# Kernel tuning notes

Hardware: AMD Instinct MI355X
Metric: run time of the kernel (lower is better)

Reference implementation:

```python
import jax, jax.numpy as jnp
import numpy as np

N_NODES = 100000
N_EDGES = 6400000
NUM_FEATURES = 128
NUM_CLASSES = 10


def _gcn_norm(edge_index, num_nodes):
    # PyG GCNConv default: add self-loops, symmetric normalization
    src, dst = edge_index[0], edge_index[1]
    loop = jnp.arange(num_nodes, dtype=src.dtype)
    src = jnp.concatenate([src, loop])
    dst = jnp.concatenate([dst, loop])
    deg = jax.ops.segment_sum(jnp.ones_like(dst, dtype=jnp.float32), dst,
                              num_segments=num_nodes)
    dinv = jnp.where(deg > 0, jax.lax.rsqrt(deg), 0.0)
    norm = dinv[src] * dinv[dst]  # [E + N]
    return src, dst, norm


def _gcn_conv(x, W, b, src, dst, norm, num_nodes):
    h = x @ W                              # [N, out] small feature matmul
    msg = h[src] * norm[:, None]           # gather + per-edge scale
    agg = jax.ops.segment_sum(msg, dst, num_segments=num_nodes)  # scatter-add
    return agg + b


def setup_inputs() -> dict:
    key = jax.random.key(0)
    ks = jax.random.split(key, 10)
    x = jax.random.normal(ks[0], (N_NODES, NUM_FEATURES), dtype=jnp.float32)
    edge_index = jax.random.randint(ks[1], (2, N_EDGES), 0, N_NODES, dtype=jnp.int64)

    def glorot(k, shape):
        lim = np.sqrt(6.0 / (shape[0] + shape[1]))
        return jax.random.uniform(k, shape, jnp.float32, -lim, lim)

    return {
        "x": x,
        "edge_index": edge_index,
        "W1": glorot(ks[2], (NUM_FEATURES, 4)), "b1": jnp.zeros((4,), jnp.float32),
        "W2": glorot(ks[3], (4, 4)),            "b2": jnp.zeros((4,), jnp.float32),
        "W3": glorot(ks[4], (4, 2)),            "b3": jnp.zeros((2,), jnp.float32),
        "Wc": glorot(ks[5], (2, NUM_CLASSES)),  "bc": jnp.zeros((NUM_CLASSES,), jnp.float32),
    }


def reference(x, edge_index, W1, b1, W2, b2, W3, b3, Wc, bc):
    num_nodes = x.shape[0]
    src, dst, norm = _gcn_norm(edge_index, num_nodes)
    h = jnp.tanh(_gcn_conv(x, W1, b1, src, dst, norm, num_nodes))
    h = jnp.tanh(_gcn_conv(h, W2, b2, src, dst, norm, num_nodes))
    h = jnp.tanh(_gcn_conv(h, W3, b3, src, dst, norm, num_nodes))
    out = h @ Wc + bc
    return out, h
```

## Files before the change

### kernel.cpp

```cpp
#include <hip/hip_runtime.h>
#include <hip/hip_bf16.h>
#include <stdint.h>

#define N_NODES 100000
#define N_EDGES 6400000

#define NPB 128
#define NBKT 782
#define CAP 10752
#define SORT_CAP 9216
#define OUT_CAP (SORT_CAP + NPB * 3)
#define BIN_CHUNK 8192
#define BIN_THREADS 512
#define BIN_ITER (BIN_CHUNK / BIN_THREADS)
#define SORT_THREADS 512
#define SORT_V4 5
#define NBIN_BLOCKS ((N_EDGES + BIN_CHUNK - 1) / BIN_CHUNK)


__device__ __forceinline__ void make_rec(unsigned s, unsigned d,
                                         unsigned& rec, short& bb) {
  if (s < N_NODES && d < N_NODES) {
    bb = (short)(d >> 7);
    rec = s | ((d & (NPB - 1u)) << 17) | (((d >> 7) & 255u) << 24);
  }
}

__global__ __launch_bounds__(512) void k_bin(const void* __restrict__ ei,
                                             int* __restrict__ gcur,
                                             unsigned* __restrict__ perm1) {
  __shared__ unsigned staging[BIN_CHUNK];
  __shared__ int lcnt[1024];
  __shared__ int wsum[8];
  __shared__ int s_tot;
  __shared__ int s_th[3];
  __shared__ int s_is64;
  int t = threadIdx.x;
  lcnt[t] = 0; lcnt[t + 512] = 0;
  if (t < 64) {
    unsigned hv = ((const unsigned*)ei)[2 * t + 1];
    unsigned long long m = __ballot(hv != 0u);
    if (t == 0) s_is64 = (m == 0ull);
  }
  __syncthreads();
  int is64 = s_is64;
  size_t e0 = (size_t)blockIdx.x * BIN_CHUNK;
  int n = (int)(((e0 + BIN_CHUNK) <= N_EDGES) ? BIN_CHUNK : (N_EDGES - e0));

  unsigned rec[BIN_ITER];
  short bb[BIN_ITER];
  short rnk[BIN_ITER];
#pragma unroll
  for (int i = 0; i < BIN_ITER; ++i) { rec[i] = 0xFFFFFFFFu; bb[i] = 0; }

  if (is64) {
    const long long* e = (const long long*)ei;
#pragma unroll
    for (int i = 0; i < BIN_ITER / 2; ++i) {
      int k = 2 * t + 1024 * i;
      if (k < n) {
        uint4 sp = *(const uint4*)(e + e0 + k);
        uint4 dp = *(const uint4*)(e + (size_t)N_EDGES + e0 + k);
        make_rec(sp.x, dp.x, rec[2 * i], bb[2 * i]);
        make_rec(sp.z, dp.z, rec[2 * i + 1], bb[2 * i + 1]);
      }
    }
  } else {
    const unsigned* e = (const unsigned*)ei;
#pragma unroll
    for (int i = 0; i < BIN_ITER / 4; ++i) {
      int k = 4 * t + 2048 * i;
      if (k < n) {
        uint4 sq = *(const uint4*)(e + e0 + k);
        uint4 dq = *(const uint4*)(e + (size_t)N_EDGES + e0 + k);
        make_rec(sq.x, dq.x, rec[4 * i],     bb[4 * i]);
        make_rec(sq.y, dq.y, rec[4 * i + 1], bb[4 * i + 1]);
        make_rec(sq.z, dq.z, rec[4 * i + 2], bb[4 * i + 2]);
        make_rec(sq.w, dq.w, rec[4 * i + 3], bb[4 * i + 3]);
      }
    }
  }
#pragma unroll
  for (int i = 0; i < BIN_ITER; ++i) {
    rnk[i] = 0;
    if (rec[i] != 0xFFFFFFFFu)
      rnk[i] = (short)atomicAdd(&lcnt[bb[i]], 1);
  }
  __syncthreads();
  int c0 = lcnt[2 * t], c1 = lcnt[2 * t + 1];
  int s = c0 + c1;
  int lane = t & 63, w = t >> 6;
  int incl = s;
#pragma unroll
  for (int o = 1; o < 64; o <<= 1) {
    int u = __shfl_up(incl, o);
    if (lane >= o) incl += u;
  }
  if (lane == 63) wsum[w] = incl;
  __syncthreads();
  int wb = 0;
  for (int i = 0; i < w; ++i) wb += wsum[i];
  int excl0 = wb + incl - s;
  int excl1 = excl0 + c0;
  lcnt[2 * t] = excl0; lcnt[2 * t + 1] = excl1;
  if (t == 128) s_th[0] = excl0;
  if (t == 256) s_th[1] = excl0;
  if (t == 384) s_th[2] = excl0;
  if (t == 511) s_tot = excl1 + c1;
  int gb0 = c0 ? atomicAdd(&gcur[2 * t], c0) : 0;
  int gb1 = c1 ? atomicAdd(&gcur[2 * t + 1], c1) : 0;
  __syncthreads();
#pragma unroll
  for (int i = 0; i < BIN_ITER; ++i) {
    if (rec[i] != 0xFFFFFFFFu) {
      int p = lcnt[bb[i]] + rnk[i];
      staging[p] = rec[i];
    }
  }
  __syncthreads();
  lcnt[2 * t] = gb0 - excl0;
  lcnt[2 * t + 1] = gb1 - excl1;
  __syncthreads();
  int tot = s_tot, th0 = s_th[0], th1 = s_th[1], th2 = s_th[2];
  for (int j = t; j < tot; j += 512) {
    unsigned r = staging[j];
    int hi = (j >= th0) + (j >= th1) + (j >= th2);
    int b = (int)(r >> 24) | (hi << 8);
    int o = lcnt[b] + j;
    if (o < CAP) perm1[(size_t)b * CAP + o] = r;
  }
}

__global__ __launch_bounds__(512) void k_sort(const int* __restrict__ gcur,
                                              const unsigned* __restrict__ perm1,
                                              unsigned* __restrict__ perm2,
                                              int2* __restrict__ offdeg,
                                              float* __restrict__ dinv) {
  __shared__ __align__(16) unsigned outbuf[OUT_CAP];
  __shared__ int h[NPB];
  __shared__ int wsum2[2];
  __shared__ int s_tot;
  int b = blockIdx.x, t = threadIdx.x;
  if (t < NPB) h[t] = 0;
  __syncthreads();
  int cnt = min(gcur[b], SORT_CAP);
  int base = b * CAP;
  unsigned rec[4 * SORT_V4];
  short rnk[4 * SORT_V4];
#pragma unroll
  for (int i = 0; i < SORT_V4; ++i) {
    int j = 4 * t + 2048 * i;
    uint4 q = *(const uint4*)(perm1 + base + j);
    rec[4 * i]     = (j     < cnt) ? q.x : 0xFFFFFFFFu;
    rec[4 * i + 1] = (j + 1 < cnt) ? q.y : 0xFFFFFFFFu;
    rec[4 * i + 2] = (j + 2 < cnt) ? q.z : 0xFFFFFFFFu;
    rec[4 * i + 3] = (j + 3 < cnt) ? q.w : 0xFFFFFFFFu;
  }
#pragma unroll
  for (int i = 0; i < 4 * SORT_V4; ++i) {
    rnk[i] = 0;
    if (rec[i] != 0xFFFFFFFFu)
      rnk[i] = (short)atomicAdd(&h[(rec[i] >> 17) & (NPB - 1)], 1);
  }
  __syncthreads();
  int degb = 0, degs4 = 0, incl = 0;
  if (t < NPB) {
    degb = h[t];
    degs4 = (degb + 3) & ~3;
    incl = degs4;
    int lane = t & 63;
#pragma unroll
    for (int o = 1; o < 64; o <<= 1) {
      int u = __shfl_up(incl, o);
      if (lane >= o) incl += u;
    }
    if (lane == 63) wsum2[t >> 6] = incl;
  }
  __syncthreads();
  int excl4 = 0;
  if (t < NPB) {
    excl4 = (t >= 64 ? wsum2[0] : 0) + incl - degs4;
    int node = b * NPB + t;
    if (node < N_NODES) {
      offdeg[node] = make_int2(base + excl4, degb);
      float dd = (float)degb + 1.0f;
      float y = rsqrtf(dd);
      y = y * (1.5f - 0.5f * dd * y * y);
      dinv[node] = y;
    }
    if (t == NPB - 1) s_tot = excl4 + degs4;
  }
  __syncthreads();
  if (t < NPB) h[t] = excl4;
  __syncthreads();
#pragma unroll
  for (int i = 0; i < 4 * SORT_V4; ++i) {
    if (rec[i] != 0xFFFFFFFFu)
      outbuf[h[(rec[i] >> 17) & (NPB - 1)] + rnk[i]] = rec[i] & 0x1FFFF;
  }
  __syncthreads();
  int tot = s_tot;
#pragma unroll
  for (int i = 0; i < SORT_V4; ++i) {
    int j = 4 * t + 2048 * i;
    if (j < tot)
      *(uint4*)(perm2 + base + j) = *(const uint4*)(outbuf + j);
  }
}

__global__ __launch_bounds__(256) void k_mm1(const float* __restrict__ x,
                                             const float* __restrict__ W1,
                                             const float* __restrict__ dinv,
                                             float* __restrict__ hs1) {
  int gid = blockIdx.x * blockDim.x + threadIdx.x;
  int node = gid >> 6;
  int lane = threadIdx.x & 63;
  if (node >= N_NODES) return;
  float2 v = ((const float2*)x)[(size_t)node * 64 + lane];
  float4 w0 = ((const float4*)W1)[2 * lane];
  float4 w1 = ((const float4*)W1)[2 * lane + 1];
  float a0 = v.x * w0.x + v.y * w1.x;
  float a1 = v.x * w0.y + v.y * w1.y;
  float a2 = v.x * w0.z + v.y * w1.z;
  float a3 = v.x * w0.w + v.y * w1.w;
#pragma unroll
  for (int off = 32; off > 0; off >>= 1) {
    a0 += __shfl_down(a0, off);
    a1 += __shfl_down(a1, off);
    a2 += __shfl_down(a2, off);
    a3 += __shfl_down(a3, off);
  }
  if (lane == 0) {
    float d = dinv[node];
    ((float4*)hs1)[node] = make_float4(d * a0, d * a1, d * a2, d * a3);
  }
}


__global__ __launch_bounds__(256) void k_l1(const int2* __restrict__ offdeg,
                                            const unsigned* __restrict__ perm2,
                                            const float* __restrict__ hs1,
                                            const float* __restrict__ dinv,
                                            const float* __restrict__ W2,
                                            const float* __restrict__ b1,
                                            float* __restrict__ hs2) {
  int node = blockIdx.x * 16 + (threadIdx.x >> 4);
  int l = threadIdx.x & 15;
  int2 od = offdeg[node];
  int base = od.x, d = od.y;
  float a0 = 0, a1 = 0, a2 = 0, a3 = 0;
  for (int j = 4 * l; j + 4 <= d; j += 64) {
    uint4 s = *(const uint4*)(perm2 + base + j);
    float4 v0 = ((const float4*)hs1)[s.x];
    float4 v1 = ((const float4*)hs1)[s.y];
    float4 v2 = ((const float4*)hs1)[s.z];
    float4 v3 = ((const float4*)hs1)[s.w];
    a0 += v0.x + v1.x + v2.x + v3.x;
    a1 += v0.y + v1.y + v2.y + v3.y;
    a2 += v0.z + v1.z + v2.z + v3.z;
    a3 += v0.w + v1.w + v2.w + v3.w;
  }
  int rb = d & ~3;
  if (l < d - rb) {
    float4 v = ((const float4*)hs1)[perm2[base + rb + l]];
    a0 += v.x; a1 += v.y; a2 += v.z; a3 += v.w;
  }
#pragma unroll
  for (int o = 8; o > 0; o >>= 1) {
    a0 += __shfl_down(a0, o); a1 += __shfl_down(a1, o);
    a2 += __shfl_down(a2, o); a3 += __shfl_down(a3, o);
  }
  if (l == 0) {
    float dn = dinv[node];
    float4 hl = ((const float4*)hs1)[node];
    float t0 = tanhf(dn * (a0 + hl.x) + b1[0]);
    float t1 = tanhf(dn * (a1 + hl.y) + b1[1]);
    float t2 = tanhf(dn * (a2 + hl.z) + b1[2]);
    float t3 = tanhf(dn * (a3 + hl.w) + b1[3]);
    float4 r;
    r.x = dn * (t0 * W2[0] + t1 * W2[4] + t2 * W2[8]  + t3 * W2[12]);
    r.y = dn * (t0 * W2[1] + t1 * W2[5] + t2 * W2[9]  + t3 * W2[13]);
    r.z = dn * (t0 * W2[2] + t1 * W2[6] + t2 * W2[10] + t3 * W2[14]);
    r.w = dn * (t0 * W2[3] + t1 * W2[7] + t2 * W2[11] + t3 * W2[15]);
    ((float4*)hs2)[node] = r;
  }
}

__global__ __launch_bounds__(256) void k_l2(const int2* __restrict__ offdeg,
                                            const unsigned* __restrict__ perm2,
                                            const float* __restrict__ hs2,
                                            const float* __restrict__ dinv,
                                            const float* __restrict__ W3,
                                            const float* __restrict__ b2,
                                            float* __restrict__ hs3) {
  int node = blockIdx.x * 16 + (threadIdx.x >> 4);
  int l = threadIdx.x & 15;
  int2 od = offdeg[node];
  int base = od.x, d = od.y;
  float a0 = 0, a1 = 0, a2 = 0, a3 = 0;
  for (int j = 4 * l; j + 4 <= d; j += 64) {
    uint4 s = *(const uint4*)(perm2 + base + j);
    float4 v0 = ((const float4*)hs2)[s.x];
    float4 v1 = ((const float4*)hs2)[s.y];
    float4 v2 = ((const float4*)hs2)[s.z];
    float4 v3 = ((const float4*)hs2)[s.w];
    a0 += v0.x + v1.x + v2.x + v3.x;
    a1 += v0.y + v1.y + v2.y + v3.y;
    a2 += v0.z + v1.z + v2.z + v3.z;
    a3 += v0.w + v1.w + v2.w + v3.w;
  }
  int rb = d & ~3;
  if (l < d - rb) {
    float4 v = ((const float4*)hs2)[perm2[base + rb + l]];
    a0 += v.x; a1 += v.y; a2 += v.z; a3 += v.w;
  }
#pragma unroll
  for (int o = 8; o > 0; o >>= 1) {
    a0 += __shfl_down(a0, o); a1 += __shfl_down(a1, o);
    a2 += __shfl_down(a2, o); a3 += __shfl_down(a3, o);
  }
  if (l == 0) {
    float dn = dinv[node];
    float4 hl = ((const float4*)hs2)[node];
    float t0 = tanhf(dn * (a0 + hl.x) + b2[0]);
    float t1 = tanhf(dn * (a1 + hl.y) + b2[1]);
    float t2 = tanhf(dn * (a2 + hl.z) + b2[2]);
    float t3 = tanhf(dn * (a3 + hl.w) + b2[3]);
    float2 r;
    r.x = dn * (t0 * W3[0] + t1 * W3[2] + t2 * W3[4] + t3 * W3[6]);
    r.y = dn * (t0 * W3[1] + t1 * W3[3] + t2 * W3[5] + t3 * W3[7]);
    ((float2*)hs3)[node] = r;
  }
}

__global__ __launch_bounds__(256) void k_l3(const int2* __restrict__ offdeg,
                                            const unsigned* __restrict__ perm2,
                                            const float* __restrict__ hs3,
                                            const float* __restrict__ dinv,
                                            const float* __restrict__ Wc,
                                            const float* __restrict__ bc,
                                            const float* __restrict__ b3,
                                            float* __restrict__ out) {
  int node = blockIdx.x * 16 + (threadIdx.x >> 4);
  int l = threadIdx.x & 15;
  int2 od = offdeg[node];
  int base = od.x, d = od.y;
  float a0 = 0, a1 = 0;
  for (int j = 4 * l; j + 4 <= d; j += 64) {
    uint4 s = *(const uint4*)(perm2 + base + j);
    float2 v0 = ((const float2*)hs3)[s.x];
    float2 v1 = ((const float2*)hs3)[s.y];
    float2 v2 = ((const float2*)hs3)[s.z];
    float2 v3 = ((const float2*)hs3)[s.w];
    a0 += v0.x + v1.x + v2.x + v3.x;
    a1 += v0.y + v1.y + v2.y + v3.y;
  }
  int rb = d & ~3;
  if (l < d - rb) {
    float2 v = ((const float2*)hs3)[perm2[base + rb + l]];
    a0 += v.x; a1 += v.y;
  }
#pragma unroll
  for (int o = 8; o > 0; o >>= 1) {
    a0 += __shfl_xor(a0, o); a1 += __shfl_xor(a1, o);
  }
  float dn = dinv[node];
  float2 hl = ((const float2*)hs3)[node];
  float t0 = tanhf(dn * (a0 + hl.x) + b3[0]);
  float t1 = tanhf(dn * (a1 + hl.y) + b3[1]);
  if (l < 10)
    out[(size_t)node * 10 + l] = t0 * Wc[l] + t1 * Wc[10 + l] + bc[l];
  else if (l == 10)
    out[(size_t)N_NODES * 10 + 2 * node + 0] = t0;
  else if (l == 11)
    out[(size_t)N_NODES * 10 + 2 * node + 1] = t1;
}

extern "C" void kernel_launch(void* const* d_in, const int* in_sizes, int n_in,
                              void* d_out, int out_size, void* d_ws, size_t ws_size,
                              hipStream_t stream) {
  const float* x  = (const float*)d_in[0];
  const void*  ei = d_in[1];
  const float* W1 = (const float*)d_in[2];
  const float* b1 = (const float*)d_in[3];
  const float* W2 = (const float*)d_in[4];
  const float* b2 = (const float*)d_in[5];
  const float* W3 = (const float*)d_in[6];
  const float* b3 = (const float*)d_in[7];
  const float* Wc = (const float*)d_in[8];
  const float* bc = (const float*)d_in[9];
  float* out = (float*)d_out;

  const size_t N = N_NODES;
  float* base = (float*)d_ws;
  float* dinv = base;
  float* hs1  = base + N;
  float* hs2  = base + 5 * N;
  float* hs3  = base + 9 * N;
  int2*  offdeg = (int2*)(base + 11 * N);
  int*   gcur = (int*)(base + 13 * N);
  unsigned* perm1 = (unsigned*)(base + 13 * N + 2048);
  unsigned* perm2 = perm1 + (size_t)NBKT * CAP;

  hipMemsetAsync(gcur, 0, 1024 * sizeof(int), stream);
  k_bin<<<NBIN_BLOCKS, BIN_THREADS, 0, stream>>>(ei, gcur, perm1);
  k_sort<<<NBKT, SORT_THREADS, 0, stream>>>(gcur, perm1, perm2, offdeg, dinv);
  k_mm1<<<(N_NODES * 64) / 256, 256, 0, stream>>>(x, W1, dinv, hs1);

  const int LB = N_NODES / 16;
  k_l1<<<LB, 256, 0, stream>>>(offdeg, perm2, hs1, dinv, W2, b1, hs2);
  k_l2<<<LB, 256, 0, stream>>>(offdeg, perm2, hs2, dinv, W3, b2, hs3);
  k_l3<<<LB, 256, 0, stream>>>(offdeg, perm2, hs3, dinv, Wc, bc, b3, out);
}
```

Before: 301.3 us.

## Halve bin chunk, pack rank into bucket word, and re-read perm1 in sort

Halves BIN_CHUNK so k_bin uses less shared memory and runs more blocks, and packs the local rank into the upper bits of the bucket index to save registers. Both kernels get a minimum-blocks hint in launch_bounds. k_sort no longer holds records and ranks in registers; it reads perm1 twice, once for the histogram and once for the scatter, and places records with atomicAdd on the offset counters. This trades extra global reads and an order-dependent placement within each node for lower register pressure and higher occupancy.

New measurement: 325.1 us. 1.08x slower.

```diff
diff --git a/kernel.cpp b/kernel.cpp
--- a/kernel.cpp
+++ b/kernel.cpp
@@ -10,7 +10,7 @@
 #define CAP 10752
 #define SORT_CAP 9216
 #define OUT_CAP (SORT_CAP + NPB * 3)
-#define BIN_CHUNK 8192
+#define BIN_CHUNK 4096
 #define BIN_THREADS 512
 #define BIN_ITER (BIN_CHUNK / BIN_THREADS)
 #define SORT_THREADS 512
@@ -19,16 +19,16 @@
 
 
 __device__ __forceinline__ void make_rec(unsigned s, unsigned d,
-                                         unsigned& rec, short& bb) {
+                                         unsigned& rec, int& pk) {
   if (s < N_NODES && d < N_NODES) {
-    bb = (short)(d >> 7);
+    pk = (int)(d >> 7);
     rec = s | ((d & (NPB - 1u)) << 17) | (((d >> 7) & 255u) << 24);
   }
 }
 
-__global__ __launch_bounds__(512) void k_bin(const void* __restrict__ ei,
-                                             int* __restrict__ gcur,
-                                             unsigned* __restrict__ perm1) {
+__global__ __launch_bounds__(512, 8) void k_bin(const void* __restrict__ ei,
+                                                int* __restrict__ gcur,
+                                                unsigned* __restrict__ perm1) {
   __shared__ unsigned staging[BIN_CHUNK];
   __shared__ int lcnt[1024];
   __shared__ int wsum[8];
@@ -48,10 +48,9 @@
   int n = (int)(((e0 + BIN_CHUNK) <= N_EDGES) ? BIN_CHUNK : (N_EDGES - e0));
 
   unsigned rec[BIN_ITER];
-  short bb[BIN_ITER];
-  short rnk[BIN_ITER];
-#pragma unroll
-  for (int i = 0; i < BIN_ITER; ++i) { rec[i] = 0xFFFFFFFFu; bb[i] = 0; }
+  int pk[BIN_ITER];
+#pragma unroll
+  for (int i = 0; i < BIN_ITER; ++i) { rec[i] = 0xFFFFFFFFu; pk[i] = 0; }
 
   if (is64) {
     const long long* e = (const long long*)ei;
@@ -61,8 +60,8 @@
       if (k < n) {
         uint4 sp = *(const uint4*)(e + e0 + k);
         uint4 dp = *(const uint4*)(e + (size_t)N_EDGES + e0 + k);
-        make_rec(sp.x, dp.x, rec[2 * i], bb[2 * i]);
-        make_rec(sp.z, dp.z, rec[2 * i + 1], bb[2 * i + 1]);
+        make_rec(sp.x, dp.x, rec[2 * i],     pk[2 * i]);
+        make_rec(sp.z, dp.z, rec[2 * i + 1], pk[2 * i + 1]);
       }
     }
   } else {
@@ -73,18 +72,19 @@
       if (k < n) {
         uint4 sq = *(const uint4*)(e + e0 + k);
         uint4 dq = *(const uint4*)(e + (size_t)N_EDGES + e0 + k);
-        make_rec(sq.x, dq.x, rec[4 * i],     bb[4 * i]);
-        make_rec(sq.y, dq.y, rec[4 * i + 1], bb[4 * i + 1]);
-        make_rec(sq.z, dq.z, rec[4 * i + 2], bb[4 * i + 2]);
-        make_rec(sq.w, dq.w, rec[4 * i + 3], bb[4 * i + 3]);
+        make_rec(sq.x, dq.x, rec[4 * i],     pk[4 * i]);
+        make_rec(sq.y, dq.y, rec[4 * i + 1], pk[4 * i + 1]);
+        make_rec(sq.z, dq.z, rec[4 * i + 2], pk[4 * i + 2]);
+        make_rec(sq.w, dq.w, rec[4 * i + 3], pk[4 * i + 3]);
       }
     }
   }
 #pragma unroll
   for (int i = 0; i < BIN_ITER; ++i) {
-    rnk[i] = 0;
-    if (rec[i] != 0xFFFFFFFFu)
-      rnk[i] = (short)atomicAdd(&lcnt[bb[i]], 1);
+    if (rec[i] != 0xFFFFFFFFu) {
+      int r = atomicAdd(&lcnt[pk[i] & 0xFFFF], 1);
+      pk[i] |= r << 16;
+    }
   }
   __syncthreads();
   int c0 = lcnt[2 * t], c1 = lcnt[2 * t + 1];
@@ -113,7 +113,7 @@
 #pragma unroll
   for (int i = 0; i < BIN_ITER; ++i) {
     if (rec[i] != 0xFFFFFFFFu) {
-      int p = lcnt[bb[i]] + rnk[i];
+      int p = lcnt[pk[i] & 0xFFFF] + (pk[i] >> 16);
       staging[p] = rec[i];
     }
   }
@@ -131,11 +131,11 @@
   }
 }
 
-__global__ __launch_bounds__(512) void k_sort(const int* __restrict__ gcur,
-                                              const unsigned* __restrict__ perm1,
-                                              unsigned* __restrict__ perm2,
-                                              int2* __restrict__ offdeg,
-                                              float* __restrict__ dinv) {
+__global__ __launch_bounds__(512, 8) void k_sort(const int* __restrict__ gcur,
+                                                 const unsigned* __restrict__ perm1,
+                                                 unsigned* __restrict__ perm2,
+                                                 int2* __restrict__ offdeg,
+                                                 float* __restrict__ dinv) {
   __shared__ __align__(16) unsigned outbuf[OUT_CAP];
   __shared__ int h[NPB];
   __shared__ int wsum2[2];
@@ -145,22 +145,16 @@
   __syncthreads();
   int cnt = min(gcur[b], SORT_CAP);
   int base = b * CAP;
-  unsigned rec[4 * SORT_V4];
-  short rnk[4 * SORT_V4];
 #pragma unroll
   for (int i = 0; i < SORT_V4; ++i) {
     int j = 4 * t + 2048 * i;
-    uint4 q = *(const uint4*)(perm1 + base + j);
-    rec[4 * i]     = (j     < cnt) ? q.x : 0xFFFFFFFFu;
-    rec[4 * i + 1] = (j + 1 < cnt) ? q.y : 0xFFFFFFFFu;
-    rec[4 * i + 2] = (j + 2 < cnt) ? q.z : 0xFFFFFFFFu;
-    rec[4 * i + 3] = (j + 3 < cnt) ? q.w : 0xFFFFFFFFu;
-  }
-#pragma unroll
-  for (int i = 0; i < 4 * SORT_V4; ++i) {
-    rnk[i] = 0;
-    if (rec[i] != 0xFFFFFFFFu)
-      rnk[i] = (short)atomicAdd(&h[(rec[i] >> 17) & (NPB - 1)], 1);
+    if (j < cnt) {
+      uint4 q = *(const uint4*)(perm1 + base + j);
+      atomicAdd(&h[(q.x >> 17) & (NPB - 1)], 1);
+      if (j + 1 < cnt) atomicAdd(&h[(q.y >> 17) & (NPB - 1)], 1);
+      if (j + 2 < cnt) atomicAdd(&h[(q.z >> 17) & (NPB - 1)], 1);
+      if (j + 3 < cnt) atomicAdd(&h[(q.w >> 17) & (NPB - 1)], 1);
+    }
   }
   __syncthreads();
   int degb = 0, degs4 = 0, incl = 0;
@@ -194,9 +188,15 @@
   if (t < NPB) h[t] = excl4;
   __syncthreads();
 #pragma unroll
-  for (int i = 0; i < 4 * SORT_V4; ++i) {
-    if (rec[i] != 0xFFFFFFFFu)
-      outbuf[h[(rec[i] >> 17) & (NPB - 1)] + rnk[i]] = rec[i] & 0x1FFFF;
+  for (int i = 0; i < SORT_V4; ++i) {
+    int j = 4 * t + 2048 * i;
+    if (j < cnt) {
+      uint4 q = *(const uint4*)(perm1 + base + j);
+      { int p = atomicAdd(&h[(q.x >> 17) & (NPB - 1)], 1); outbuf[p] = q.x & 0x1FFFF; }
+      if (j + 1 < cnt) { int p = atomicAdd(&h[(q.y >> 17) & (NPB - 1)], 1); outbuf[p] = q.y & 0x1FFFF; }
+      if (j + 2 < cnt) { int p = atomicAdd(&h[(q.z >> 17) & (NPB - 1)], 1); outbuf[p] = q.z & 0x1FFFF; }
+      if (j + 3 < cnt) { int p = atomicAdd(&h[(q.w >> 17) & (NPB - 1)], 1); outbuf[p] = q.w & 0x1FFFF; }
+    }
   }
   __syncthreads();
   int tot = s_tot;
```

## Two-pass binning: count then re-read edges, doubling chunk size per block

Applied to the files above, without the earlier changes.

The binning kernel no longer keeps per-edge records and ranks in registers. It reads each edge chunk twice: one pass counts per-bucket histograms, the second re-reads the edges and claims slots through shared atomics on prefix offsets. The chunk per block doubles to 16384 edges, which halves the number of blocks and the global atomics on bucket cursors, and fewer registers are needed. The costs are a second global read of the edge indices, twice the shared staging memory (64KB, which may reduce occupancy), and a non-deterministic order within each bucket.

Result: faster. 286.9 us (-4.8%).

```diff
diff --git a/kernel.cpp b/kernel.cpp
--- a/kernel.cpp
+++ b/kernel.cpp
@@ -10,27 +10,19 @@
 #define CAP 10752
 #define SORT_CAP 9216
 #define OUT_CAP (SORT_CAP + NPB * 3)
-#define BIN_CHUNK 8192
+#define BIN_CHUNK 16384
 #define BIN_THREADS 512
-#define BIN_ITER (BIN_CHUNK / BIN_THREADS)
 #define SORT_THREADS 512
 #define SORT_V4 5
 #define NBIN_BLOCKS ((N_EDGES + BIN_CHUNK - 1) / BIN_CHUNK)
 
-
-__device__ __forceinline__ void make_rec(unsigned s, unsigned d,
-                                         unsigned& rec, short& bb) {
-  if (s < N_NODES && d < N_NODES) {
-    bb = (short)(d >> 7);
-    rec = s | ((d & (NPB - 1u)) << 17) | (((d >> 7) & 255u) << 24);
-  }
-}
 
 __global__ __launch_bounds__(512) void k_bin(const void* __restrict__ ei,
                                              int* __restrict__ gcur,
                                              unsigned* __restrict__ perm1) {
   __shared__ unsigned staging[BIN_CHUNK];
   __shared__ int lcnt[1024];
+  __shared__ int combo[1024];
   __shared__ int wsum[8];
   __shared__ int s_tot;
   __shared__ int s_th[3];
@@ -47,44 +39,24 @@
   size_t e0 = (size_t)blockIdx.x * BIN_CHUNK;
   int n = (int)(((e0 + BIN_CHUNK) <= N_EDGES) ? BIN_CHUNK : (N_EDGES - e0));
 
-  unsigned rec[BIN_ITER];
-  short bb[BIN_ITER];
-  short rnk[BIN_ITER];
-#pragma unroll
-  for (int i = 0; i < BIN_ITER; ++i) { rec[i] = 0xFFFFFFFFu; bb[i] = 0; }
-
   if (is64) {
     const long long* e = (const long long*)ei;
-#pragma unroll
-    for (int i = 0; i < BIN_ITER / 2; ++i) {
-      int k = 2 * t + 1024 * i;
-      if (k < n) {
-        uint4 sp = *(const uint4*)(e + e0 + k);
-        uint4 dp = *(const uint4*)(e + (size_t)N_EDGES + e0 + k);
-        make_rec(sp.x, dp.x, rec[2 * i], bb[2 * i]);
-        make_rec(sp.z, dp.z, rec[2 * i + 1], bb[2 * i + 1]);
-      }
+    for (int k = 2 * t; k < n; k += 1024) {
+      uint4 sp = *(const uint4*)(e + e0 + k);
+      uint4 dp = *(const uint4*)(e + (size_t)N_EDGES + e0 + k);
+      if (sp.x < N_NODES && dp.x < N_NODES) atomicAdd(&lcnt[dp.x >> 7], 1);
+      if (sp.z < N_NODES && dp.z < N_NODES) atomicAdd(&lcnt[dp.z >> 7], 1);
     }
   } else {
     const unsigned* e = (const unsigned*)ei;
-#pragma unroll
-    for (int i = 0; i < BIN_ITER / 4; ++i) {
-      int k = 4 * t + 2048 * i;
-      if (k < n) {
-        uint4 sq = *(const uint4*)(e + e0 + k);
-        uint4 dq = *(const uint4*)(e + (size_t)N_EDGES + e0 + k);
-        make_rec(sq.x, dq.x, rec[4 * i],     bb[4 * i]);
-        make_rec(sq.y, dq.y, rec[4 * i + 1], bb[4 * i + 1]);
-        make_rec(sq.z, dq.z, rec[4 * i + 2], bb[4 * i + 2]);
-        make_rec(sq.w, dq.w, rec[4 * i + 3], bb[4 * i + 3]);
-      }
-    }
-  }
-#pragma unroll
-  for (int i = 0; i < BIN_ITER; ++i) {
-    rnk[i] = 0;
-    if (rec[i] != 0xFFFFFFFFu)
-      rnk[i] = (short)atomicAdd(&lcnt[bb[i]], 1);
+    for (int k = 4 * t; k < n; k += 2048) {
+      uint4 sq = *(const uint4*)(e + e0 + k);
+      uint4 dq = *(const uint4*)(e + (size_t)N_EDGES + e0 + k);
+      if (sq.x < N_NODES && dq.x < N_NODES) atomicAdd(&lcnt[dq.x >> 7], 1);
+      if (sq.y < N_NODES && dq.y < N_NODES) atomicAdd(&lcnt[dq.y >> 7], 1);
+      if (sq.z < N_NODES && dq.z < N_NODES) atomicAdd(&lcnt[dq.z >> 7], 1);
+      if (sq.w < N_NODES && dq.w < N_NODES) atomicAdd(&lcnt[dq.w >> 7], 1);
+    }
   }
   __syncthreads();
   int c0 = lcnt[2 * t], c1 = lcnt[2 * t + 1];
@@ -102,31 +74,60 @@
   for (int i = 0; i < w; ++i) wb += wsum[i];
   int excl0 = wb + incl - s;
   int excl1 = excl0 + c0;
+  int gb0 = c0 ? atomicAdd(&gcur[2 * t], c0) : 0;
+  int gb1 = c1 ? atomicAdd(&gcur[2 * t + 1], c1) : 0;
   lcnt[2 * t] = excl0; lcnt[2 * t + 1] = excl1;
+  combo[2 * t] = gb0 - excl0;
+  combo[2 * t + 1] = gb1 - excl1;
   if (t == 128) s_th[0] = excl0;
   if (t == 256) s_th[1] = excl0;
   if (t == 384) s_th[2] = excl0;
   if (t == 511) s_tot = excl1 + c1;
-  int gb0 = c0 ? atomicAdd(&gcur[2 * t], c0) : 0;
-  int gb1 = c1 ? atomicAdd(&gcur[2 * t + 1], c1) : 0;
-  __syncthreads();
-#pragma unroll
-  for (int i = 0; i < BIN_ITER; ++i) {
-    if (rec[i] != 0xFFFFFFFFu) {
-      int p = lcnt[bb[i]] + rnk[i];
-      staging[p] = rec[i];
-    }
-  }
-  __syncthreads();
-  lcnt[2 * t] = gb0 - excl0;
-  lcnt[2 * t + 1] = gb1 - excl1;
+  __syncthreads();
+  if (is64) {
+    const long long* e = (const long long*)ei;
+    for (int k = 2 * t; k < n; k += 1024) {
+      uint4 sp = *(const uint4*)(e + e0 + k);
+      uint4 dp = *(const uint4*)(e + (size_t)N_EDGES + e0 + k);
+      if (sp.x < N_NODES && dp.x < N_NODES) {
+        int p = atomicAdd(&lcnt[dp.x >> 7], 1);
+        staging[p] = sp.x | ((dp.x & (NPB - 1u)) << 17) | (((dp.x >> 7) & 255u) << 24);
+      }
+      if (sp.z < N_NODES && dp.z < N_NODES) {
+        int p = atomicAdd(&lcnt[dp.z >> 7], 1);
+        staging[p] = sp.z | ((dp.z & (NPB - 1u)) << 17) | (((dp.z >> 7) & 255u) << 24);
+      }
+    }
+  } else {
+    const unsigned* e = (const unsigned*)ei;
+    for (int k = 4 * t; k < n; k += 2048) {
+      uint4 sq = *(const uint4*)(e + e0 + k);
+      uint4 dq = *(const uint4*)(e + (size_t)N_EDGES + e0 + k);
+      if (sq.x < N_NODES && dq.x < N_NODES) {
+        int p = atomicAdd(&lcnt[dq.x >> 7], 1);
+        staging[p] = sq.x | ((dq.x & (NPB - 1u)) << 17) | (((dq.x >> 7) & 255u) << 24);
+      }
+      if (sq.y < N_NODES && dq.y < N_NODES) {
+        int p = atomicAdd(&lcnt[dq.y >> 7], 1);
+        staging[p] = sq.y | ((dq.y & (NPB - 1u)) << 17) | (((dq.y >> 7) & 255u) << 24);
+      }
+      if (sq.z < N_NODES && dq.z < N_NODES) {
+        int p = atomicAdd(&lcnt[dq.z >> 7], 1);
+        staging[p] = sq.z | ((dq.z & (NPB - 1u)) << 17) | (((dq.z >> 7) & 255u) << 24);
+      }
+      if (sq.w < N_NODES && dq.w < N_NODES) {
+        int p = atomicAdd(&lcnt[dq.w >> 7], 1);
+        staging[p] = sq.w | ((dq.w & (NPB - 1u)) << 17) | (((dq.w >> 7) & 255u) << 24);
+      }
+    }
+  }
   __syncthreads();
   int tot = s_tot, th0 = s_th[0], th1 = s_th[1], th2 = s_th[2];
   for (int j = t; j < tot; j += 512) {
     unsigned r = staging[j];
     int hi = (j >= th0) + (j >= th1) + (j >= th2);
     int b = (int)(r >> 24) | (hi << 8);
-    int o = lcnt[b] + j;
+    int o = combo[b] + j;
     if (o < CAP) perm1[(size_t)b * CAP + o] = r;
   }
 }
```
